# Kernel optimization log

Hardware: AMD Instinct MI355X
Metric: run time of the kernel (lower is better)

Reference implementation:

```python
import jax, jax.numpy as jnp
import numpy as np

B, S, HID, H, D = 4, 1024, 1024, 16, 64
MAXP = 1024  # max_position_embeddings
EPS = 1e-8


def setup_inputs() -> dict:
    key = jax.random.key(0)
    ks = jax.random.split(key, 9)
    scale = 0.02  # keep logits small since masked_softmax has no max-subtraction
    return {
        "hidden_states": jax.random.normal(ks[0], (B, S, HID), jnp.float32),
        "attention_mask": jnp.zeros((B, 1, 1, S), jnp.float32),
        "skim_mask": jax.random.randint(ks[1], (B, S), 0, 2, jnp.int32),
        "Wq": jax.random.normal(ks[2], (HID, HID), jnp.float32) * scale,
        "bq": jnp.zeros((HID,), jnp.float32),
        "Wk": jax.random.normal(ks[3], (HID, HID), jnp.float32) * scale,
        "bk": jnp.zeros((HID,), jnp.float32),
        "Wv": jax.random.normal(ks[4], (HID, HID), jnp.float32) * scale,
        "bv": jnp.zeros((HID,), jnp.float32),
        "dist_emb": jax.random.normal(ks[5], (2 * MAXP - 1, D), jnp.float32) * scale,
    }


def reference(hidden_states, attention_mask, skim_mask, Wq, bq, Wk, bk, Wv, bv, dist_emb):
    # Linear projections (W stored as [in, out]) then split heads: [B,H,S,D]
    def heads(x):
        return x.reshape(B, S, H, D).transpose(0, 2, 1, 3)

    q = heads(hidden_states @ Wq + bq)
    k = heads(hidden_states @ Wk + bk)
    v = heads(hidden_states @ Wv + bv)

    # raw scores [B,H,S,S]
    scores = jnp.einsum('bhld,bhrd->bhlr', q, k)

    # relative_key positional bias
    pos = jnp.arange(S)
    distance = pos[:, None] - pos[None, :]                 # [S,S]
    pe = dist_emb[distance + MAXP - 1]                     # [S,S,D]
    scores = scores + jnp.einsum('bhld,lrd->bhlr', q, pe)

    scores = scores / jnp.sqrt(jnp.float32(D))
    scores = scores + attention_mask

    # skim_mask branch: masked_softmax (exp * mask, normalized with eps)
    mask = skim_mask[:, None, None, :].astype(scores.dtype)  # [B,1,1,S]
    exps = jnp.exp(scores) * mask
    probs = exps / (EPS + exps.sum(-1, keepdims=True))
    # dropout in eval mode -> identity

    ctx = jnp.einsum('bhlr,bhrd->bhld', probs, v)
    return ctx.transpose(0, 2, 1, 3).reshape(B, S, HID)
```

## Files before the change

kernel.cpp:

```cpp
#include <hip/hip_runtime.h>
#include <hip/hip_bf16.h>


#define EPSV 1e-8f

typedef short bfrag __attribute__((ext_vector_type(8)));
typedef float cfrag __attribute__((ext_vector_type(16)));
typedef int v2i __attribute__((ext_vector_type(2)));

__device__ __forceinline__ short f2bf(float f) {
    __hip_bfloat16 h = __float2bfloat16(f);
    return *reinterpret_cast<short*>(&h);
}
__device__ __forceinline__ float bf2f(short s) {
    unsigned int u = ((unsigned int)(unsigned short)s) << 16;
    return __builtin_bit_cast(float, u);
}
__device__ __forceinline__ unsigned int pk2(short a, short b) {
    return (unsigned int)(unsigned short)a | ((unsigned int)(unsigned short)b << 16);
}

__global__ __launch_bounds__(256) void prep(
    const float* __restrict__ hidden, const float* __restrict__ Wq,
    const float* __restrict__ Wk, const float* __restrict__ Wv,
    const float* __restrict__ dist,
    short* __restrict__ Xs, short* __restrict__ Wt, short* __restrict__ Db)
{
    __shared__ short Tl[32 * 72];
    const int bid = blockIdx.x, tid = threadIdx.x;

    if (bid < 2048) {
        const int mt = bid >> 4, kg = bid & 15;
        const int m_l = tid >> 3, k8 = (tid & 7) * 8;
        const float* src = hidden + (size_t)(mt * 32 + m_l) * 1024 + kg * 64 + k8;
        float4 v0 = *(const float4*)src, v1 = *(const float4*)(src + 4);
        short o[8];
        o[0] = f2bf(v0.x); o[1] = f2bf(v0.y); o[2] = f2bf(v0.z); o[3] = f2bf(v0.w);
        o[4] = f2bf(v1.x); o[5] = f2bf(v1.y); o[6] = f2bf(v1.z); o[7] = f2bf(v1.w);
        *(bfrag*)&Tl[m_l * 72 + k8] = *(bfrag*)o;
        __syncthreads();
        const int l31 = tid & 31, q2 = (tid >> 5) & 1, kc = tid >> 6;
        bfrag r = *(const bfrag*)&Tl[l31 * 72 + kc * 16 + q2 * 8];
        *(bfrag*)(Xs + ((size_t)(mt * 64 + kg * 4 + kc) * 64 + q2 * 32 + l31) * 8) = r;
    } else if (bid < 3584) {
        const int t = bid - 2048, z = t >> 9, nt = (t >> 4) & 31, kg = t & 15;
        const float* W = (z == 0) ? Wq : ((z == 1) ? Wk : Wv);
        const int k_l = tid >> 2, n8 = (tid & 3) * 8;
        const float* src = W + (size_t)(kg * 64 + k_l) * 1024 + nt * 32 + n8;
        float4 v0 = *(const float4*)src, v1 = *(const float4*)(src + 4);
        float vv[8] = {v0.x, v0.y, v0.z, v0.w, v1.x, v1.y, v1.z, v1.w};
#pragma unroll
        for (int i = 0; i < 8; i++)
            Tl[(n8 + i) * 72 + k_l] = f2bf(vv[i]);
        __syncthreads();
        const int l31 = tid & 31, q2 = (tid >> 5) & 1, kc = tid >> 6;
        bfrag r = *(const bfrag*)&Tl[l31 * 72 + kc * 16 + q2 * 8];
        *(bfrag*)(Wt + (size_t)z * 1048576
                  + ((size_t)(nt * 64 + kg * 4 + kc) * 64 + q2 * 32 + l31) * 8) = r;
    } else {
        const int idx = (bid - 3584) * 256 + tid;
        if (idx < 16376) {
            const float* src = dist + (size_t)idx * 8;
            float4 v0 = *(const float4*)src, v1 = *(const float4*)(src + 4);
            short o[8];
            o[0] = f2bf(v0.x); o[1] = f2bf(v0.y); o[2] = f2bf(v0.z); o[3] = f2bf(v0.w);
            o[4] = f2bf(v1.x); o[5] = f2bf(v1.y); o[6] = f2bf(v1.z); o[7] = f2bf(v1.w);
            *(bfrag*)(Db + (size_t)idx * 8) = *(bfrag*)o;
        }
    }
}

__global__ __launch_bounds__(256) void qkv_mfma(
    const short* __restrict__ Xs, const short* __restrict__ Wt,
    const float* __restrict__ bq, const float* __restrict__ bk,
    const float* __restrict__ bv,
    short* __restrict__ Qf, short* __restrict__ Kf, short* __restrict__ Vt)
{
    const int z = blockIdx.z;
    const short* W = Wt + (size_t)z * 1048576;
    const float* bias = (z == 0) ? bq : ((z == 1) ? bk : bv);
    const float scale = (z == 0) ? 0.18033688011112042f : 1.0f;

    const int tid = threadIdx.x, lane = tid & 63, wid = tid >> 6;
    const int q2 = lane >> 5, l31 = lane & 31;
    const int wr = wid >> 1, wc = wid & 1;
    const int m0 = blockIdx.x * 128, n0 = blockIdx.y * 128;

    cfrag acc[2][2];
#pragma unroll
    for (int i = 0; i < 2; i++)
#pragma unroll
        for (int j = 0; j < 2; j++)
#pragma unroll
            for (int e = 0; e < 16; e++) acc[i][j][e] = 0.f;

    const short* ap0 = Xs + ((size_t)((m0 >> 5) + wr * 2 + 0) * 64 * 64 + lane) * 8;
    const short* ap1 = Xs + ((size_t)((m0 >> 5) + wr * 2 + 1) * 64 * 64 + lane) * 8;
    const short* bp0 = W  + ((size_t)((n0 >> 5) + wc * 2 + 0) * 64 * 64 + lane) * 8;
    const short* bp1 = W  + ((size_t)((n0 >> 5) + wc * 2 + 1) * 64 * 64 + lane) * 8;

#pragma unroll 4
    for (int kc = 0; kc < 64; kc++) {
        const int off = kc * 512;
        bfrag a0 = *(const bfrag*)(ap0 + off);
        bfrag a1 = *(const bfrag*)(ap1 + off);
        bfrag b0 = *(const bfrag*)(bp0 + off);
        bfrag b1 = *(const bfrag*)(bp1 + off);
        acc[0][0] = __builtin_amdgcn_mfma_f32_32x32x16_bf16(a0, b0, acc[0][0], 0, 0, 0);
        acc[0][1] = __builtin_amdgcn_mfma_f32_32x32x16_bf16(a0, b1, acc[0][1], 0, 0, 0);
        acc[1][0] = __builtin_amdgcn_mfma_f32_32x32x16_bf16(a1, b0, acc[1][0], 0, 0, 0);
        acc[1][1] = __builtin_amdgcn_mfma_f32_32x32x16_bf16(a1, b1, acc[1][1], 0, 0, 0);
    }

#pragma unroll
    for (int nt = 0; nt < 2; nt++) {
        const int c = n0 + wc * 64 + nt * 32 + l31;
        const float bval = bias[c];
        const int h = c >> 6;
        const int d = nt * 32 + l31;
#pragma unroll
        for (int mt = 0; mt < 2; mt++) {
            const int tok0 = m0 + wr * 64 + mt * 32;
            const int bb = tok0 >> 10, s_base = tok0 & 1023;
            const size_t bhbase = (size_t)(bb * 16 + h) * 65536;
            if (z < 2) {
                short* outp = (z == 0) ? Qf : Kf;
                const size_t fbase = bhbase
                    + ((size_t)((s_base >> 5) * 4 + (d >> 4)) * 64
                       + ((d >> 3) & 1) * 32) * 8 + (d & 7);
#pragma unroll
                for (int reg = 0; reg < 16; reg++) {
                    const int row = (reg & 3) + 8 * (reg >> 2) + 4 * q2;
                    outp[fbase + (size_t)row * 8] = f2bf((acc[mt][nt][reg] + bval) * scale);
                }
            } else {
#pragma unroll
                for (int g = 0; g < 4; g++) {
                    const float e0 = acc[mt][nt][4 * g + 0] + bval;
                    const float e1 = acc[mt][nt][4 * g + 1] + bval;
                    const float e2 = acc[mt][nt][4 * g + 2] + bval;
                    const float e3 = acc[mt][nt][4 * g + 3] + bval;
                    uint2 w2;
                    w2.x = pk2(f2bf(e0), f2bf(e1));
                    w2.y = pk2(f2bf(e2), f2bf(e3));
                    const size_t flat = bhbase
                        + ((size_t)(nt * 64 + (s_base >> 4) + (g >> 1)) * 64
                           + (g & 1) * 32 + l31) * 8 + 4 * q2;
                    *(uint2*)(Vt + flat) = w2;
                }
            }
        }
    }
}

__global__ __launch_bounds__(256, 2) void attn_mfma(
    const short* __restrict__ Qf, const short* __restrict__ Kf,
    const short* __restrict__ Vt, const short* __restrict__ Db,
    const float* __restrict__ amask, const int* __restrict__ skim,
    float* __restrict__ out)
{
    __shared__ short Tb[128 * 132];
    __shared__ float Lg[1024];

    const int tid = threadIdx.x, lane = tid & 63, w = tid >> 6;
    const int q2 = lane >> 5, l31 = lane & 31;
    const int bh = blockIdx.x, b = bh >> 4, hh = bh & 15;
    const int l0 = blockIdx.y * 128;

    {
        const int r4 = tid * 4;
        float4 am = *(const float4*)(amask + b * 1024 + r4);
        int4 sk = *(const int4*)(skim + b * 1024 + r4);
        Lg[r4 + 0] = __expf(am.x) * (float)sk.x;
        Lg[r4 + 1] = __expf(am.y) * (float)sk.y;
        Lg[r4 + 2] = __expf(am.z) * (float)sk.z;
        Lg[r4 + 3] = __expf(am.w) * (float)sk.w;
    }
    __syncthreads();

    const short* Qg = Qf + (size_t)bh * 65536;
    const short* Kg = Kf + (size_t)bh * 65536;
    const short* Vg = Vt + (size_t)bh * 65536;

    bfrag qa[4];
#pragma unroll
    for (int c = 0; c < 4; c++)
        qa[c] = *(const bfrag*)(Qg + ((size_t)(((l0 >> 5) + w) * 4 + c) * 64 + lane) * 8);

    cfrag oacc[2];
#pragma unroll
    for (int mt = 0; mt < 2; mt++)
#pragma unroll
        for (int e = 0; e < 16; e++) oacc[mt][e] = 0.f;
    float es[4] = {0.f, 0.f, 0.f, 0.f};

    const int Lband = l0 + 32 * w;
    const int lg = Lband + l31;
    const int rowb = (32 * w + l31) * 132;

    for (int r0 = -128; r0 < 1024; r0 += 64) {
        const bool produce = r0 < 960;

        bfrag pb[2][4];
        if (produce) {
#pragma unroll
            for (int mt = 0; mt < 2; mt++) {
                const int D0 = Lband - r0 - 128 + 32 * mt;
                const int er = min(max(D0 + l31 + 1023, 0), 2046);
#pragma unroll
                for (int kc = 0; kc < 4; kc++)
                    pb[mt][kc] = *(const bfrag*)(Db + (size_t)er * 64 + kc * 16 + q2 * 8);
            }
        }

        if (r0 >= 0) {
            bfrag kb[2][4], vbl[4][2];
#pragma unroll
            for (int mt = 0; mt < 2; mt++)
#pragma unroll
                for (int kc = 0; kc < 4; kc++)
                    kb[mt][kc] = *(const bfrag*)(Kg
                        + ((size_t)(((r0 >> 5) + mt) * 4 + kc) * 64 + lane) * 8);
#pragma unroll
            for (int kc = 0; kc < 4; kc++)
#pragma unroll
                for (int mtd = 0; mtd < 2; mtd++)
                    vbl[kc][mtd] = *(const bfrag*)(Vg
                        + ((size_t)(mtd * 64 + (r0 >> 4) + kc) * 64 + lane) * 8);

#pragma unroll
            for (int mt = 0; mt < 2; mt++) {
                cfrag sfr;
#pragma unroll
                for (int e = 0; e < 16; e++) sfr[e] = 0.f;
#pragma unroll
                for (int kc = 0; kc < 4; kc++)
                    sfr = __builtin_amdgcn_mfma_f32_32x32x16_bf16(
                        kb[mt][kc], qa[kc], sfr, 0, 0, 0);

                unsigned int P[4][2];
#pragma unroll
                for (int g = 0; g < 4; g++) {
                    const int rb = r0 + 32 * mt + 8 * g + 4 * q2;
                    float4 g4 = *(const float4*)&Lg[rb];
                    v2i tr = *(const v2i*)&Tb[rowb + (rb & 127)];
                    const float tv0 = __builtin_bit_cast(float, (unsigned)tr[0] << 16);
                    const float tv1 = __builtin_bit_cast(float, (unsigned)tr[0] & 0xffff0000u);
                    const float tv2 = __builtin_bit_cast(float, (unsigned)tr[1] << 16);
                    const float tv3 = __builtin_bit_cast(float, (unsigned)tr[1] & 0xffff0000u);
                    float ev0 = __builtin_amdgcn_exp2f(sfr[4 * g + 0] + tv0) * g4.x;
                    float ev1 = __builtin_amdgcn_exp2f(sfr[4 * g + 1] + tv1) * g4.y;
                    float ev2 = __builtin_amdgcn_exp2f(sfr[4 * g + 2] + tv2) * g4.z;
                    float ev3 = __builtin_amdgcn_exp2f(sfr[4 * g + 3] + tv3) * g4.w;
                    es[0] += ev0; es[1] += ev1; es[2] += ev2; es[3] += ev3;
                    P[g][0] = pk2(f2bf(ev0), f2bf(ev1));
                    P[g][1] = pk2(f2bf(ev2), f2bf(ev3));
                }
#pragma unroll
                for (int c = 0; c < 2; c++) {
                    v2i s0 = __builtin_amdgcn_permlane32_swap(
                        (int)P[2 * c][0], (int)P[2 * c + 1][0], false, false);
                    v2i s1 = __builtin_amdgcn_permlane32_swap(
                        (int)P[2 * c][1], (int)P[2 * c + 1][1], false, false);
                    union { bfrag f; int d[4]; } u;
                    u.d[0] = s0[0]; u.d[1] = s1[0]; u.d[2] = s0[1]; u.d[3] = s1[1];
                    const int kc = 2 * mt + c;
#pragma unroll
                    for (int mtd = 0; mtd < 2; mtd++)
                        oacc[mtd] = __builtin_amdgcn_mfma_f32_32x32x16_bf16(
                            vbl[kc][mtd], u.f, oacc[mtd], 0, 0, 0);
                }
            }
        }

        if (produce) {
#pragma unroll
            for (int mt = 0; mt < 2; mt++) {
                cfrag t;
#pragma unroll
                for (int e = 0; e < 16; e++) t[e] = 0.f;
#pragma unroll
                for (int kc = 0; kc < 4; kc++)
                    t = __builtin_amdgcn_mfma_f32_32x32x16_bf16(
                        pb[mt][kc], qa[kc], t, 0, 0, 0);
#pragma unroll
                for (int e = 0; e < 16; e++) {
                    const int rr = (e & 3) + 8 * (e >> 2) + 4 * q2;
                    Tb[rowb + ((l31 + r0 - 32 * mt - rr) & 127)] = f2bf(t[e]);
                }
            }
        }
    }

    float esum = (es[0] + es[1]) + (es[2] + es[3]);
    const float den = EPSV + esum + __shfl_xor(esum, 32);
    const float inv = 1.0f / den;
    float* ob = out + ((size_t)(b * 1024 + lg) * 1024) + hh * 64;
#pragma unroll
    for (int mtd = 0; mtd < 2; mtd++) {
#pragma unroll
        for (int g = 0; g < 4; g++) {
            float4 o;
            o.x = oacc[mtd][4 * g + 0] * inv;
            o.y = oacc[mtd][4 * g + 1] * inv;
            o.z = oacc[mtd][4 * g + 2] * inv;
            o.w = oacc[mtd][4 * g + 3] * inv;
            *(float4*)(ob + 32 * mtd + 8 * g + 4 * q2) = o;
        }
    }
}

extern "C" void kernel_launch(void* const* d_in, const int* in_sizes, int n_in,
                              void* d_out, int out_size, void* d_ws, size_t ws_size,
                              hipStream_t stream) {
    const float* hidden = (const float*)d_in[0];
    const float* amask  = (const float*)d_in[1];
    const int*   skim   = (const int*)d_in[2];
    const float* Wq     = (const float*)d_in[3];
    const float* bq     = (const float*)d_in[4];
    const float* Wk     = (const float*)d_in[5];
    const float* bk     = (const float*)d_in[6];
    const float* Wv     = (const float*)d_in[7];
    const float* bv     = (const float*)d_in[8];
    const float* dist   = (const float*)d_in[9];
    float* out = (float*)d_out;

    char* w = (char*)d_ws;
    short* Xs  = (short*)(w);
    short* Wt  = (short*)(w + ((size_t)8 << 20));
    short* Db  = (short*)(w + ((size_t)14 << 20));
    short* Qf  = (short*)(w + ((size_t)15 << 20));
    short* Kf  = (short*)(w + ((size_t)23 << 20));
    short* Vt  = (short*)(w + ((size_t)31 << 20));

    prep<<<3648, 256, 0, stream>>>(hidden, Wq, Wk, Wv, dist, Xs, Wt, Db);
    qkv_mfma<<<dim3(32, 8, 3), 256, 0, stream>>>(Xs, Wt, bq, bk, bv, Qf, Kf, Vt);
    attn_mfma<<<dim3(64, 8), 256, 0, stream>>>(Qf, Kf, Vt, Db, amask, skim, out);
}
```

Before: 196.2 us.

## Double-buffer GEMM loads, seed score MFMA with bias, add setprio around MFMAs

The projection GEMM now uses register double-buffering, loading the next k-chunk's fragments before issuing MFMAs on the current ones. In attention, the relative-position bias tile is loaded from LDS up front and used as the initial accumulator for the QK MFMA, which removes separate adds before exp2. MFMA blocks are wrapped in s_setprio to favor matrix issue across waves, and the exp sums are kept in packed float2 accumulators. Together these aim to hide load latency and trim VALU work, at the cost of more live registers and possibly lower occupancy.

```diff
diff --git a/kernel.cpp b/kernel.cpp
--- a/kernel.cpp
+++ b/kernel.cpp
@@ -7,14 +7,11 @@
 typedef short bfrag __attribute__((ext_vector_type(8)));
 typedef float cfrag __attribute__((ext_vector_type(16)));
 typedef int v2i __attribute__((ext_vector_type(2)));
+typedef float v2f __attribute__((ext_vector_type(2)));
 
 __device__ __forceinline__ short f2bf(float f) {
     __hip_bfloat16 h = __float2bfloat16(f);
     return *reinterpret_cast<short*>(&h);
-}
-__device__ __forceinline__ float bf2f(short s) {
-    unsigned int u = ((unsigned int)(unsigned short)s) << 16;
-    return __builtin_bit_cast(float, u);
 }
 __device__ __forceinline__ unsigned int pk2(short a, short b) {
     return (unsigned int)(unsigned short)a | ((unsigned int)(unsigned short)b << 16);
@@ -99,17 +96,30 @@
     const short* bp0 = W  + ((size_t)((n0 >> 5) + wc * 2 + 0) * 64 * 64 + lane) * 8;
     const short* bp1 = W  + ((size_t)((n0 >> 5) + wc * 2 + 1) * 64 * 64 + lane) * 8;
 
-#pragma unroll 4
-    for (int kc = 0; kc < 64; kc++) {
-        const int off = kc * 512;
-        bfrag a0 = *(const bfrag*)(ap0 + off);
-        bfrag a1 = *(const bfrag*)(ap1 + off);
-        bfrag b0 = *(const bfrag*)(bp0 + off);
-        bfrag b1 = *(const bfrag*)(bp1 + off);
-        acc[0][0] = __builtin_amdgcn_mfma_f32_32x32x16_bf16(a0, b0, acc[0][0], 0, 0, 0);
-        acc[0][1] = __builtin_amdgcn_mfma_f32_32x32x16_bf16(a0, b1, acc[0][1], 0, 0, 0);
-        acc[1][0] = __builtin_amdgcn_mfma_f32_32x32x16_bf16(a1, b0, acc[1][0], 0, 0, 0);
-        acc[1][1] = __builtin_amdgcn_mfma_f32_32x32x16_bf16(a1, b1, acc[1][1], 0, 0, 0);
+    bfrag a0c, a1c, b0c, b1c, a0n, a1n, b0n, b1n;
+    a0c = *(const bfrag*)(ap0); a1c = *(const bfrag*)(ap1);
+    b0c = *(const bfrag*)(bp0); b1c = *(const bfrag*)(bp1);
+
+#pragma unroll 2
+    for (int kc = 0; kc < 64; kc += 2) {
+        {
+            const int off = (kc + 1) * 512;
+            a0n = *(const bfrag*)(ap0 + off); a1n = *(const bfrag*)(ap1 + off);
+            b0n = *(const bfrag*)(bp0 + off); b1n = *(const bfrag*)(bp1 + off);
+        }
+        acc[0][0] = __builtin_amdgcn_mfma_f32_32x32x16_bf16(a0c, b0c, acc[0][0], 0, 0, 0);
+        acc[0][1] = __builtin_amdgcn_mfma_f32_32x32x16_bf16(a0c, b1c, acc[0][1], 0, 0, 0);
+        acc[1][0] = __builtin_amdgcn_mfma_f32_32x32x16_bf16(a1c, b0c, acc[1][0], 0, 0, 0);
+        acc[1][1] = __builtin_amdgcn_mfma_f32_32x32x16_bf16(a1c, b1c, acc[1][1], 0, 0, 0);
+        if (kc + 2 < 64) {
+            const int off = (kc + 2) * 512;
+            a0c = *(const bfrag*)(ap0 + off); a1c = *(const bfrag*)(ap1 + off);
+            b0c = *(const bfrag*)(bp0 + off); b1c = *(const bfrag*)(bp1 + off);
+        }
+        acc[0][0] = __builtin_amdgcn_mfma_f32_32x32x16_bf16(a0n, b0n, acc[0][0], 0, 0, 0);
+        acc[0][1] = __builtin_amdgcn_mfma_f32_32x32x16_bf16(a0n, b1n, acc[0][1], 0, 0, 0);
+        acc[1][0] = __builtin_amdgcn_mfma_f32_32x32x16_bf16(a1n, b0n, acc[1][0], 0, 0, 0);
+        acc[1][1] = __builtin_amdgcn_mfma_f32_32x32x16_bf16(a1n, b1n, acc[1][1], 0, 0, 0);
     }
 
 #pragma unroll
@@ -192,7 +202,7 @@
     for (int mt = 0; mt < 2; mt++)
 #pragma unroll
         for (int e = 0; e < 16; e++) oacc[mt][e] = 0.f;
-    float es[4] = {0.f, 0.f, 0.f, 0.f};
+    v2f es01 = {0.f, 0.f}, es23 = {0.f, 0.f};
 
     const int Lband = l0 + 32 * w;
     const int lg = Lband + l31;
@@ -215,6 +225,7 @@
 
         if (r0 >= 0) {
             bfrag kb[2][4], vbl[4][2];
+            v2i trr[2][4];
 #pragma unroll
             for (int mt = 0; mt < 2; mt++)
 #pragma unroll
@@ -227,32 +238,42 @@
                 for (int mtd = 0; mtd < 2; mtd++)
                     vbl[kc][mtd] = *(const bfrag*)(Vg
                         + ((size_t)(mtd * 64 + (r0 >> 4) + kc) * 64 + lane) * 8);
+#pragma unroll
+            for (int mt = 0; mt < 2; mt++)
+#pragma unroll
+                for (int g = 0; g < 4; g++)
+                    trr[mt][g] = *(const v2i*)&Tb[rowb
+                        + ((r0 + 32 * mt + 8 * g + 4 * q2) & 127)];
 
 #pragma unroll
             for (int mt = 0; mt < 2; mt++) {
                 cfrag sfr;
 #pragma unroll
-                for (int e = 0; e < 16; e++) sfr[e] = 0.f;
+                for (int g = 0; g < 4; g++) {
+                    const v2i t2 = trr[mt][g];
+                    sfr[4 * g + 0] = __builtin_bit_cast(float, (unsigned)t2[0] << 16);
+                    sfr[4 * g + 1] = __builtin_bit_cast(float, (unsigned)t2[0] & 0xffff0000u);
+                    sfr[4 * g + 2] = __builtin_bit_cast(float, (unsigned)t2[1] << 16);
+                    sfr[4 * g + 3] = __builtin_bit_cast(float, (unsigned)t2[1] & 0xffff0000u);
+                }
+                __builtin_amdgcn_s_setprio(1);
 #pragma unroll
                 for (int kc = 0; kc < 4; kc++)
                     sfr = __builtin_amdgcn_mfma_f32_32x32x16_bf16(
                         kb[mt][kc], qa[kc], sfr, 0, 0, 0);
+                __builtin_amdgcn_s_setprio(0);
 
                 unsigned int P[4][2];
 #pragma unroll
                 for (int g = 0; g < 4; g++) {
                     const int rb = r0 + 32 * mt + 8 * g + 4 * q2;
                     float4 g4 = *(const float4*)&Lg[rb];
-                    v2i tr = *(const v2i*)&Tb[rowb + (rb & 127)];
-                    const float tv0 = __builtin_bit_cast(float, (unsigned)tr[0] << 16);
-                    const float tv1 = __builtin_bit_cast(float, (unsigned)tr[0] & 0xffff0000u);
-                    const float tv2 = __builtin_bit_cast(float, (unsigned)tr[1] << 16);
-                    const float tv3 = __builtin_bit_cast(float, (unsigned)tr[1] & 0xffff0000u);
-                    float ev0 = __builtin_amdgcn_exp2f(sfr[4 * g + 0] + tv0) * g4.x;
-                    float ev1 = __builtin_amdgcn_exp2f(sfr[4 * g + 1] + tv1) * g4.y;
-                    float ev2 = __builtin_amdgcn_exp2f(sfr[4 * g + 2] + tv2) * g4.z;
-                    float ev3 = __builtin_amdgcn_exp2f(sfr[4 * g + 3] + tv3) * g4.w;
-                    es[0] += ev0; es[1] += ev1; es[2] += ev2; es[3] += ev3;
+                    float ev0 = __builtin_amdgcn_exp2f(sfr[4 * g + 0]) * g4.x;
+                    float ev1 = __builtin_amdgcn_exp2f(sfr[4 * g + 1]) * g4.y;
+                    float ev2 = __builtin_amdgcn_exp2f(sfr[4 * g + 2]) * g4.z;
+                    float ev3 = __builtin_amdgcn_exp2f(sfr[4 * g + 3]) * g4.w;
+                    es01 += (v2f){ev0, ev1};
+                    es23 += (v2f){ev2, ev3};
                     P[g][0] = pk2(f2bf(ev0), f2bf(ev1));
                     P[g][1] = pk2(f2bf(ev2), f2bf(ev3));
                 }
@@ -265,10 +286,12 @@
                     union { bfrag f; int d[4]; } u;
                     u.d[0] = s0[0]; u.d[1] = s1[0]; u.d[2] = s0[1]; u.d[3] = s1[1];
                     const int kc = 2 * mt + c;
+                    __builtin_amdgcn_s_setprio(1);
 #pragma unroll
                     for (int mtd = 0; mtd < 2; mtd++)
                         oacc[mtd] = __builtin_amdgcn_mfma_f32_32x32x16_bf16(
                             vbl[kc][mtd], u.f, oacc[mtd], 0, 0, 0);
+                    __builtin_amdgcn_s_setprio(0);
                 }
             }
         }
@@ -279,10 +302,12 @@
                 cfrag t;
 #pragma unroll
                 for (int e = 0; e < 16; e++) t[e] = 0.f;
+                __builtin_amdgcn_s_setprio(1);
 #pragma unroll
                 for (int kc = 0; kc < 4; kc++)
                     t = __builtin_amdgcn_mfma_f32_32x32x16_bf16(
                         pb[mt][kc], qa[kc], t, 0, 0, 0);
+                __builtin_amdgcn_s_setprio(0);
 #pragma unroll
                 for (int e = 0; e < 16; e++) {
                     const int rr = (e & 3) + 8 * (e >> 2) + 4 * q2;
@@ -292,7 +317,7 @@
         }
     }
 
-    float esum = (es[0] + es[1]) + (es[2] + es[3]);
+    float esum = (es01[0] + es01[1]) + (es23[0] + es23[1]);
     const float den = EPSV + esum + __shfl_xor(esum, 32);
     const float inv = 1.0f / den;
     float* ob = out + ((size_t)(b * 1024 + lg) * 1024) + hh * 64;
```

Result: faster. 187.1 us (-4.6%).
